# Kernel tuning notes

Hardware: AMD Instinct MI355X
Metric: run time of the kernel (lower is better)

## Reference

```python
import jax, jax.numpy as jnp
import numpy as np

USER_NUM = 100000
ITEM_NUM = 100000
EMB = 128
N_USERS = 65536
N_BEH = 2097152
N_GROUPS = 2048


def setup_inputs() -> dict:
    key = jax.random.key(0)
    ks = jax.random.split(key, 7)
    user_ids = jax.random.randint(ks[0], (N_USERS,), 0, USER_NUM, dtype=jnp.int32)
    user_group_ids = jnp.sort(jax.random.randint(ks[1], (N_USERS,), 0, N_GROUPS, dtype=jnp.int32))
    behavior_item_ids = jax.random.randint(ks[2], (N_BEH,), 0, ITEM_NUM, dtype=jnp.int32)
    behavior_counts = jax.random.uniform(ks[3], (N_BEH,), dtype=jnp.float32)
    behavior_user_ids = jnp.sort(jax.random.randint(ks[4], (N_BEH,), 0, N_USERS, dtype=jnp.int32))
    user_table = jax.random.normal(ks[5], (USER_NUM, EMB), dtype=jnp.float32)
    item_table = jax.random.normal(ks[6], (ITEM_NUM, EMB), dtype=jnp.float32)
    return {
        "user_ids": user_ids,
        "user_group_ids": user_group_ids,
        "behavior_item_ids": behavior_item_ids,
        "behavior_counts": behavior_counts,
        "behavior_user_ids": behavior_user_ids,
        "user_table": user_table,
        "item_table": item_table,
        "num_groups": N_GROUPS,
    }


def reference(user_ids, user_group_ids, behavior_item_ids, behavior_counts,
              behavior_user_ids, user_table, item_table, num_groups):
    n_users = user_ids.shape[0]
    # weighted bag-of-items per user: sum_j item_emb[b_id] * count  -> [n_users, EMB]
    beh_emb = item_table[behavior_item_ids] * behavior_counts[:, None]
    per_user_beh = jax.ops.segment_sum(beh_emb, behavior_user_ids, num_segments=n_users)
    # user embedding with padding_idx=0 (id 0 -> zero vector)
    ue = user_table[user_ids] * (user_ids != 0).astype(user_table.dtype)[:, None]
    per_user = per_user_beh * ue  # personalized behavior embedding
    # pooling == 'sum' over users within each group -> [num_groups, EMB]
    group_embedding = jax.ops.segment_sum(per_user, user_group_ids, num_segments=num_groups)
    return group_embedding
```

## Files before the change

kernel.cpp:

```cpp
#include <hip/hip_runtime.h>
#include <hip/hip_fp16.h>

#define EMB 128

__global__ __launch_bounds__(256) void prep_kernel(
    const float* __restrict__ src, __half* __restrict__ dst, int n8,
    const int* __restrict__ beh_user, int* __restrict__ start,
    int n_beh, int n_users)
{
    int t = blockIdx.x * 256 + threadIdx.x;
    if (t < n8) {
        const float4* s = (const float4*)src + (size_t)t * 2;
        float4 f0 = s[0];
        float4 f1 = s[1];
        union { __half h[8]; uint4 u; } pk;
        pk.h[0] = __float2half_rn(f0.x); pk.h[1] = __float2half_rn(f0.y);
        pk.h[2] = __float2half_rn(f0.z); pk.h[3] = __float2half_rn(f0.w);
        pk.h[4] = __float2half_rn(f1.x); pk.h[5] = __float2half_rn(f1.y);
        pk.h[6] = __float2half_rn(f1.z); pk.h[7] = __float2half_rn(f1.w);
        ((uint4*)dst)[t] = pk.u;
    }
    if (t < n_beh) {
        int cur  = beh_user[t];
        int prev = (t == 0) ? -1 : beh_user[t - 1];
        if (cur != prev) {
            for (int u = prev + 1; u <= cur; ++u) start[u] = t;
        }
        if (t == n_beh - 1) {
            for (int u = cur + 1; u <= n_users; ++u) start[u] = n_beh;
        }
    }
}

#define ACCUM(W_, c)                                              \
    {                                                             \
        float2 f01 = __half22float2(*(const __half2*)&(W_).x);    \
        float2 f23 = __half22float2(*(const __half2*)&(W_).y);    \
        float2 f45 = __half22float2(*(const __half2*)&(W_).z);    \
        float2 f67 = __half22float2(*(const __half2*)&(W_).w);    \
        a0 = fmaf(f01.x, (c), a0); a1 = fmaf(f01.y, (c), a1);     \
        a2 = fmaf(f23.x, (c), a2); a3 = fmaf(f23.y, (c), a3);     \
        a4 = fmaf(f45.x, (c), a4); a5 = fmaf(f45.y, (c), a5);     \
        a6 = fmaf(f67.x, (c), a6); a7 = fmaf(f67.y, (c), a7);     \
    }

__global__ __launch_bounds__(256) void per_user_kernel(
    const int*    __restrict__ user_ids,
    const int*    __restrict__ group_ids,
    const int*    __restrict__ beh_item,
    const float*  __restrict__ beh_cnt,
    const float*  __restrict__ user_table,
    const __half* __restrict__ item_f16,
    const int*    __restrict__ start,
    float*        __restrict__ out,
    int n_users)
{
    const int lane = threadIdx.x & 63;
    const int q    = lane >> 4;
    const int r    = lane & 15;
    const int wave = threadIdx.x >> 6;
    const int user = blockIdx.x * 4 + wave;

    __shared__ float lds_acc[EMB];
    __shared__ int   lds_grp[4];
    if (threadIdx.x < EMB) lds_acc[threadIdx.x] = 0.0f;

    float a0 = 0.f, a1 = 0.f, a2 = 0.f, a3 = 0.f;
    float a4 = 0.f, a5 = 0.f, a6 = 0.f, a7 = 0.f;
    int g = -1;

    if (user < n_users) {
        const int s = start[user];
        const int e = start[user + 1];
        g = group_ids[user];

        if (s < e) {
            const __half* itp = item_f16 + r * 8;

            int   idx0 = 0; float cnt0 = 0.f;
            {
                int t0 = s + r;
                if (t0 < e) { idx0 = __builtin_nontemporal_load(beh_item + t0);
                              cnt0 = __builtin_nontemporal_load(beh_cnt + t0); }
            }
            int   idxN = 0; float cntN = 0.f;
            {
                int t1 = s + 16 + r;
                if (t1 < e) { idxN = __builtin_nontemporal_load(beh_item + t1);
                              cntN = __builtin_nontemporal_load(beh_cnt + t1); }
            }
            int   bi0 = __shfl(idx0, q * 4 + 0, 16);
            int   bi1 = __shfl(idx0, q * 4 + 1, 16);
            int   bi2 = __shfl(idx0, q * 4 + 2, 16);
            int   bi3 = __shfl(idx0, q * 4 + 3, 16);
            float cc0 = __shfl(cnt0, q * 4 + 0, 16);
            float cc1 = __shfl(cnt0, q * 4 + 1, 16);
            float cc2 = __shfl(cnt0, q * 4 + 2, 16);
            float cc3 = __shfl(cnt0, q * 4 + 3, 16);
            uint4 wc0 = *(const uint4*)(itp + (size_t)bi0 * EMB);
            uint4 wc1 = *(const uint4*)(itp + (size_t)bi1 * EMB);
            uint4 wc2 = *(const uint4*)(itp + (size_t)bi2 * EMB);
            uint4 wc3 = *(const uint4*)(itp + (size_t)bi3 * EMB);

            #pragma unroll 2
            for (int j = s; ; ) {
                int   idx2 = 0; float cnt2 = 0.f;
                {
                    int t2 = j + 32 + r;
                    if (t2 < e) { idx2 = __builtin_nontemporal_load(beh_item + t2);
                                  cnt2 = __builtin_nontemporal_load(beh_cnt + t2); }
                }
                int   ni0 = __shfl(idxN, q * 4 + 0, 16);
                int   ni1 = __shfl(idxN, q * 4 + 1, 16);
                int   ni2 = __shfl(idxN, q * 4 + 2, 16);
                int   ni3 = __shfl(idxN, q * 4 + 3, 16);
                float nc0 = __shfl(cntN, q * 4 + 0, 16);
                float nc1 = __shfl(cntN, q * 4 + 1, 16);
                float nc2 = __shfl(cntN, q * 4 + 2, 16);
                float nc3 = __shfl(cntN, q * 4 + 3, 16);
                uint4 wn0 = *(const uint4*)(itp + (size_t)ni0 * EMB);
                uint4 wn1 = *(const uint4*)(itp + (size_t)ni1 * EMB);
                uint4 wn2 = *(const uint4*)(itp + (size_t)ni2 * EMB);
                uint4 wn3 = *(const uint4*)(itp + (size_t)ni3 * EMB);

                ACCUM(wc0, cc0);
                ACCUM(wc1, cc1);
                ACCUM(wc2, cc2);
                ACCUM(wc3, cc3);

                j += 16;
                if (j >= e) break;

                wc0 = wn0; wc1 = wn1; wc2 = wn2; wc3 = wn3;
                cc0 = nc0; cc1 = nc1; cc2 = nc2; cc3 = nc3;
                idxN = idx2; cntN = cnt2;
            }
        }

        a0 += __shfl_xor(a0, 16, 64); a1 += __shfl_xor(a1, 16, 64);
        a2 += __shfl_xor(a2, 16, 64); a3 += __shfl_xor(a3, 16, 64);
        a4 += __shfl_xor(a4, 16, 64); a5 += __shfl_xor(a5, 16, 64);
        a6 += __shfl_xor(a6, 16, 64); a7 += __shfl_xor(a7, 16, 64);
        a0 += __shfl_xor(a0, 32, 64); a1 += __shfl_xor(a1, 32, 64);
        a2 += __shfl_xor(a2, 32, 64); a3 += __shfl_xor(a3, 32, 64);
        a4 += __shfl_xor(a4, 32, 64); a5 += __shfl_xor(a5, 32, 64);
        a6 += __shfl_xor(a6, 32, 64); a7 += __shfl_xor(a7, 32, 64);

        const int uid = user_ids[user];
        if (uid != 0) {
            const float* up = user_table + (size_t)uid * EMB + r * 8;
            a0 *= __builtin_nontemporal_load(up + 0);
            a1 *= __builtin_nontemporal_load(up + 1);
            a2 *= __builtin_nontemporal_load(up + 2);
            a3 *= __builtin_nontemporal_load(up + 3);
            a4 *= __builtin_nontemporal_load(up + 4);
            a5 *= __builtin_nontemporal_load(up + 5);
            a6 *= __builtin_nontemporal_load(up + 6);
            a7 *= __builtin_nontemporal_load(up + 7);
        } else {
            a0 = a1 = a2 = a3 = a4 = a5 = a6 = a7 = 0.f;
        }
    }

    float v0, v1;
    if      (q == 0) { v0 = a0; v1 = a1; }
    else if (q == 1) { v0 = a2; v1 = a3; }
    else if (q == 2) { v0 = a4; v1 = a5; }
    else             { v0 = a6; v1 = a7; }
    const int d0 = r * 8 + q * 2;

    if (lane == 0) lds_grp[wave] = g;
    __syncthreads();

    const int g0 = lds_grp[0];
    const bool same = (g0 >= 0) && (lds_grp[1] == g0) &&
                      (lds_grp[2] == g0) && (lds_grp[3] == g0);
    if (same) {
        atomicAdd(&lds_acc[d0],     v0);
        atomicAdd(&lds_acc[d0 + 1], v1);
        __syncthreads();
        if (threadIdx.x < 64) {
            const int d = threadIdx.x * 2;
            atomicAdd(&out[(size_t)g0 * EMB + d],     lds_acc[d]);
            atomicAdd(&out[(size_t)g0 * EMB + d + 1], lds_acc[d + 1]);
        }
    } else if (g >= 0) {
        atomicAdd(&out[(size_t)g * EMB + d0],     v0);
        atomicAdd(&out[(size_t)g * EMB + d0 + 1], v1);
    }
}

__global__ __launch_bounds__(256) void per_user_f32_kernel(
    const int*   __restrict__ user_ids,
    const int*   __restrict__ group_ids,
    const int*   __restrict__ beh_item,
    const float* __restrict__ beh_cnt,
    const int*   __restrict__ beh_user,
    const float* __restrict__ user_table,
    const float* __restrict__ item_f32,
    float*       __restrict__ out,
    int n_users, int n_beh)
{
    const int lane = threadIdx.x & 63;
    const int wave = threadIdx.x >> 6;
    const int user = blockIdx.x * 4 + wave;
    float2 acc = make_float2(0.f, 0.f);
    int g = -1;
    if (user < n_users) {
        int lo = 0, hi = n_beh;
        while (lo < hi) { int m = (lo + hi) >> 1; if (beh_user[m] < user) lo = m + 1; else hi = m; }
        int s = lo; hi = n_beh;
        while (lo < hi) { int m = (lo + hi) >> 1; if (beh_user[m] <= user) lo = m + 1; else hi = m; }
        int e = lo;
        for (int j = s; j < e; ++j) {
            int   b = beh_item[j];
            float c = beh_cnt[j];
            float2 v = *(const float2*)(item_f32 + (size_t)b * EMB + lane * 2);
            acc.x = fmaf(v.x, c, acc.x);
            acc.y = fmaf(v.y, c, acc.y);
        }
        int uid = user_ids[user];
        float2 ue = make_float2(0.f, 0.f);
        if (uid != 0) ue = *(const float2*)(user_table + (size_t)uid * EMB + lane * 2);
        acc.x *= ue.x; acc.y *= ue.y;
        g = group_ids[user];
    }
    if (g >= 0) {
        atomicAdd(&out[(size_t)g * EMB + lane * 2],     acc.x);
        atomicAdd(&out[(size_t)g * EMB + lane * 2 + 1], acc.y);
    }
}

extern "C" void kernel_launch(void* const* d_in, const int* in_sizes, int n_in,
                              void* d_out, int out_size, void* d_ws, size_t ws_size,
                              hipStream_t stream) {
    const int*   user_ids   = (const int*)  d_in[0];
    const int*   group_ids  = (const int*)  d_in[1];
    const int*   beh_item   = (const int*)  d_in[2];
    const float* beh_cnt    = (const float*)d_in[3];
    const int*   beh_user   = (const int*)  d_in[4];
    const float* user_table = (const float*)d_in[5];
    const float* item_table = (const float*)d_in[6];

    const int n_users = in_sizes[0];
    const int n_beh   = in_sizes[2];
    const int item_n  = in_sizes[6] / EMB;

    float* out = (float*)d_out;
    (void)hipMemsetAsync(out, 0, (size_t)out_size * sizeof(float), stream);

    size_t start_bytes = (size_t)(n_users + 1) * sizeof(int);
    size_t f16_off     = (start_bytes + 255) & ~(size_t)255;
    size_t f16_bytes   = (size_t)item_n * EMB * sizeof(__half);

    if (ws_size < f16_off + f16_bytes) {
        int ublocks = (n_users + 3) / 4;
        per_user_f32_kernel<<<ublocks, 256, 0, stream>>>(
            user_ids, group_ids, beh_item, beh_cnt, beh_user,
            user_table, item_table, out, n_users, n_beh);
        return;
    }

    int*    start    = (int*)d_ws;
    __half* item_f16 = (__half*)((char*)d_ws + f16_off);

    int n8 = (item_n * EMB) / 8;
    int prep_n = n8 > n_beh ? n8 : n_beh;
    prep_kernel<<<(prep_n + 255) / 256, 256, 0, stream>>>(
        item_table, item_f16, n8, beh_user, start, n_beh, n_users);

    int ublocks = (n_users + 3) / 4;
    per_user_kernel<<<ublocks, 256, 0, stream>>>(
        user_ids, group_ids, beh_item, beh_cnt,
        user_table, item_f16, start, out, n_users);
}
```

Before: 224.4 us.

## Split embedding dimension across four blocks per user group in per-user kernel

Each group of four users is now handled by four blocks, each covering a 32-wide slice of the 128-dim embedding. Each lane loads 4 halves (8 bytes) per item instead of 16 bytes, and handles 2 items per step instead of 4, with an extra shuffle-reduction stage. The aim is more parallelism and fewer registers per thread. In exchange, behavior indices, counts and start offsets are re-read four times, and gathers get narrower.

```diff
diff --git a/kernel.cpp b/kernel.cpp
--- a/kernel.cpp
+++ b/kernel.cpp
@@ -36,12 +36,8 @@
     {                                                             \
         float2 f01 = __half22float2(*(const __half2*)&(W_).x);    \
         float2 f23 = __half22float2(*(const __half2*)&(W_).y);    \
-        float2 f45 = __half22float2(*(const __half2*)&(W_).z);    \
-        float2 f67 = __half22float2(*(const __half2*)&(W_).w);    \
         a0 = fmaf(f01.x, (c), a0); a1 = fmaf(f01.y, (c), a1);     \
         a2 = fmaf(f23.x, (c), a2); a3 = fmaf(f23.y, (c), a3);     \
-        a4 = fmaf(f45.x, (c), a4); a5 = fmaf(f45.y, (c), a5);     \
-        a6 = fmaf(f67.x, (c), a6); a7 = fmaf(f67.y, (c), a7);     \
     }
 
 __global__ __launch_bounds__(256) void per_user_kernel(
@@ -56,17 +52,18 @@
     int n_users)
 {
     const int lane = threadIdx.x & 63;
-    const int q    = lane >> 4;
-    const int r    = lane & 15;
+    const int oct  = lane >> 3;
+    const int p    = lane & 7;
+    const int r16  = lane & 15;
     const int wave = threadIdx.x >> 6;
-    const int user = blockIdx.x * 4 + wave;
-
-    __shared__ float lds_acc[EMB];
+    const int db   = blockIdx.x & 3;
+    const int user = (blockIdx.x >> 2) * 4 + wave;
+
+    __shared__ float lds_acc[32];
     __shared__ int   lds_grp[4];
-    if (threadIdx.x < EMB) lds_acc[threadIdx.x] = 0.0f;
+    if (threadIdx.x < 32) lds_acc[threadIdx.x] = 0.0f;
 
     float a0 = 0.f, a1 = 0.f, a2 = 0.f, a3 = 0.f;
-    float a4 = 0.f, a5 = 0.f, a6 = 0.f, a7 = 0.f;
     int g = -1;
 
     if (user < n_users) {
@@ -75,99 +72,69 @@
         g = group_ids[user];
 
         if (s < e) {
-            const __half* itp = item_f16 + r * 8;
+            const __half* itp = item_f16 + db * 32 + p * 4;
 
             int   idx0 = 0; float cnt0 = 0.f;
             {
-                int t0 = s + r;
+                int t0 = s + r16;
                 if (t0 < e) { idx0 = __builtin_nontemporal_load(beh_item + t0);
                               cnt0 = __builtin_nontemporal_load(beh_cnt + t0); }
             }
             int   idxN = 0; float cntN = 0.f;
             {
-                int t1 = s + 16 + r;
+                int t1 = s + 16 + r16;
                 if (t1 < e) { idxN = __builtin_nontemporal_load(beh_item + t1);
                               cntN = __builtin_nontemporal_load(beh_cnt + t1); }
             }
-            int   bi0 = __shfl(idx0, q * 4 + 0, 16);
-            int   bi1 = __shfl(idx0, q * 4 + 1, 16);
-            int   bi2 = __shfl(idx0, q * 4 + 2, 16);
-            int   bi3 = __shfl(idx0, q * 4 + 3, 16);
-            float cc0 = __shfl(cnt0, q * 4 + 0, 16);
-            float cc1 = __shfl(cnt0, q * 4 + 1, 16);
-            float cc2 = __shfl(cnt0, q * 4 + 2, 16);
-            float cc3 = __shfl(cnt0, q * 4 + 3, 16);
-            uint4 wc0 = *(const uint4*)(itp + (size_t)bi0 * EMB);
-            uint4 wc1 = *(const uint4*)(itp + (size_t)bi1 * EMB);
-            uint4 wc2 = *(const uint4*)(itp + (size_t)bi2 * EMB);
-            uint4 wc3 = *(const uint4*)(itp + (size_t)bi3 * EMB);
+            int   bi0 = __shfl(idx0, oct,     64);
+            int   bi1 = __shfl(idx0, 8 + oct, 64);
+            float cc0 = __shfl(cnt0, oct,     64);
+            float cc1 = __shfl(cnt0, 8 + oct, 64);
+            uint2 wc0 = *(const uint2*)(itp + (size_t)bi0 * EMB);
+            uint2 wc1 = *(const uint2*)(itp + (size_t)bi1 * EMB);
 
             #pragma unroll 2
             for (int j = s; ; ) {
                 int   idx2 = 0; float cnt2 = 0.f;
                 {
-                    int t2 = j + 32 + r;
+                    int t2 = j + 32 + r16;
                     if (t2 < e) { idx2 = __builtin_nontemporal_load(beh_item + t2);
                                   cnt2 = __builtin_nontemporal_load(beh_cnt + t2); }
                 }
-                int   ni0 = __shfl(idxN, q * 4 + 0, 16);
-                int   ni1 = __shfl(idxN, q * 4 + 1, 16);
-                int   ni2 = __shfl(idxN, q * 4 + 2, 16);
-                int   ni3 = __shfl(idxN, q * 4 + 3, 16);
-                float nc0 = __shfl(cntN, q * 4 + 0, 16);
-                float nc1 = __shfl(cntN, q * 4 + 1, 16);
-                float nc2 = __shfl(cntN, q * 4 + 2, 16);
-                float nc3 = __shfl(cntN, q * 4 + 3, 16);
-                uint4 wn0 = *(const uint4*)(itp + (size_t)ni0 * EMB);
-                uint4 wn1 = *(const uint4*)(itp + (size_t)ni1 * EMB);
-                uint4 wn2 = *(const uint4*)(itp + (size_t)ni2 * EMB);
-                uint4 wn3 = *(const uint4*)(itp + (size_t)ni3 * EMB);
+                int   ni0 = __shfl(idxN, oct,     64);
+                int   ni1 = __shfl(idxN, 8 + oct, 64);
+                float nc0 = __shfl(cntN, oct,     64);
+                float nc1 = __shfl(cntN, 8 + oct, 64);
+                uint2 wn0 = *(const uint2*)(itp + (size_t)ni0 * EMB);
+                uint2 wn1 = *(const uint2*)(itp + (size_t)ni1 * EMB);
 
                 ACCUM(wc0, cc0);
                 ACCUM(wc1, cc1);
-                ACCUM(wc2, cc2);
-                ACCUM(wc3, cc3);
 
                 j += 16;
                 if (j >= e) break;
 
-                wc0 = wn0; wc1 = wn1; wc2 = wn2; wc3 = wn3;
-                cc0 = nc0; cc1 = nc1; cc2 = nc2; cc3 = nc3;
+                wc0 = wn0; wc1 = wn1;
+                cc0 = nc0; cc1 = nc1;
                 idxN = idx2; cntN = cnt2;
             }
         }
 
+        a0 += __shfl_xor(a0,  8, 64); a1 += __shfl_xor(a1,  8, 64);
+        a2 += __shfl_xor(a2,  8, 64); a3 += __shfl_xor(a3,  8, 64);
         a0 += __shfl_xor(a0, 16, 64); a1 += __shfl_xor(a1, 16, 64);
         a2 += __shfl_xor(a2, 16, 64); a3 += __shfl_xor(a3, 16, 64);
-        a4 += __shfl_xor(a4, 16, 64); a5 += __shfl_xor(a5, 16, 64);
-        a6 += __shfl_xor(a6, 16, 64); a7 += __shfl_xor(a7, 16, 64);
         a0 += __shfl_xor(a0, 32, 64); a1 += __shfl_xor(a1, 32, 64);
         a2 += __shfl_xor(a2, 32, 64); a3 += __shfl_xor(a3, 32, 64);
-        a4 += __shfl_xor(a4, 32, 64); a5 += __shfl_xor(a5, 32, 64);
-        a6 += __shfl_xor(a6, 32, 64); a7 += __shfl_xor(a7, 32, 64);
 
         const int uid = user_ids[user];
         if (uid != 0) {
-            const float* up = user_table + (size_t)uid * EMB + r * 8;
-            a0 *= __builtin_nontemporal_load(up + 0);
-            a1 *= __builtin_nontemporal_load(up + 1);
-            a2 *= __builtin_nontemporal_load(up + 2);
-            a3 *= __builtin_nontemporal_load(up + 3);
-            a4 *= __builtin_nontemporal_load(up + 4);
-            a5 *= __builtin_nontemporal_load(up + 5);
-            a6 *= __builtin_nontemporal_load(up + 6);
-            a7 *= __builtin_nontemporal_load(up + 7);
+            float4 ue = *(const float4*)(user_table + (size_t)uid * EMB + db * 32 + p * 4);
+            a0 *= ue.x; a1 *= ue.y; a2 *= ue.z; a3 *= ue.w;
         } else {
-            a0 = a1 = a2 = a3 = a4 = a5 = a6 = a7 = 0.f;
-        }
-    }
-
-    float v0, v1;
-    if      (q == 0) { v0 = a0; v1 = a1; }
-    else if (q == 1) { v0 = a2; v1 = a3; }
-    else if (q == 2) { v0 = a4; v1 = a5; }
-    else             { v0 = a6; v1 = a7; }
-    const int d0 = r * 8 + q * 2;
+            a0 = a1 = a2 = a3 = 0.f;
+        }
+    }
 
     if (lane == 0) lds_grp[wave] = g;
     __syncthreads();
@@ -176,17 +143,22 @@
     const bool same = (g0 >= 0) && (lds_grp[1] == g0) &&
                       (lds_grp[2] == g0) && (lds_grp[3] == g0);
     if (same) {
-        atomicAdd(&lds_acc[d0],     v0);
-        atomicAdd(&lds_acc[d0 + 1], v1);
+        if (oct == 0) {
+            atomicAdd(&lds_acc[p * 4 + 0], a0);
+            atomicAdd(&lds_acc[p * 4 + 1], a1);
+            atomicAdd(&lds_acc[p * 4 + 2], a2);
+            atomicAdd(&lds_acc[p * 4 + 3], a3);
+        }
         __syncthreads();
-        if (threadIdx.x < 64) {
-            const int d = threadIdx.x * 2;
-            atomicAdd(&out[(size_t)g0 * EMB + d],     lds_acc[d]);
-            atomicAdd(&out[(size_t)g0 * EMB + d + 1], lds_acc[d + 1]);
-        }
-    } else if (g >= 0) {
-        atomicAdd(&out[(size_t)g * EMB + d0],     v0);
-        atomicAdd(&out[(size_t)g * EMB + d0 + 1], v1);
+        if (threadIdx.x < 32) {
+            atomicAdd(&out[(size_t)g0 * EMB + db * 32 + threadIdx.x],
+                      lds_acc[threadIdx.x]);
+        }
+    } else if (g >= 0 && oct == 0) {
+        atomicAdd(&out[(size_t)g * EMB + db * 32 + p * 4 + 0], a0);
+        atomicAdd(&out[(size_t)g * EMB + db * 32 + p * 4 + 1], a1);
+        atomicAdd(&out[(size_t)g * EMB + db * 32 + p * 4 + 2], a2);
+        atomicAdd(&out[(size_t)g * EMB + db * 32 + p * 4 + 3], a3);
     }
 }
 
@@ -270,7 +242,7 @@
         item_table, item_f16, n8, beh_user, start, n_beh, n_users);
 
     int ublocks = (n_users + 3) / 4;
-    per_user_kernel<<<ublocks, 256, 0, stream>>>(
+    per_user_kernel<<<ublocks * 4, 256, 0, stream>>>(
         user_ids, group_ids, beh_item, beh_cnt,
         user_table, item_f16, start, out, n_users);
 }
```

After: 304.0 us. 35.5% more time.
